# Kernel tuning notes

Hardware: AMD Instinct MI355X
Metric: run time of the kernel (lower is better)

## Reference

```python
import jax, jax.numpy as jnp
import numpy as np

B, L, LH, D, H = 32, 512, 2048, 1024, 4
DK = D // H  # dot-attn head dim
NEG = -1e9


def _ln(x, g, b, eps=1e-5):
    m = x.mean(-1, keepdims=True)
    v = ((x - m) ** 2).mean(-1, keepdims=True)
    return (x - m) / jnp.sqrt(v + eps) * g + b


def setup_inputs() -> dict:
    key = jax.random.key(0)
    ks = jax.random.split(key, 16)
    s = 0.05
    inp = {
        "seq_emb": jax.random.normal(ks[0], (B, L, D), jnp.float32),
        "seq_mask": jnp.ones((B, L), jnp.float32),
        "his_seq_emb": jax.random.normal(ks[1], (B, LH, D), jnp.float32),
        "his_seq_mask": jnp.ones((B, LH), jnp.float32),
        # dot-product MHA (bias=True)
        "sa_wq": jax.random.normal(ks[2], (D, D), jnp.float32) * s,
        "sa_bq": jnp.zeros((D,), jnp.float32),
        "sa_wk": jax.random.normal(ks[3], (D, D), jnp.float32) * s,
        "sa_bk": jnp.zeros((D,), jnp.float32),
        "sa_wv": jax.random.normal(ks[4], (D, D), jnp.float32) * s,
        "sa_bv": jnp.zeros((D,), jnp.float32),
        "sa_wo": jax.random.normal(ks[5], (D, D), jnp.float32) * s,
        "sa_bo": jnp.zeros((D,), jnp.float32),
        # short LayerNorm
        "sn_g": jnp.ones((D,), jnp.float32),
        "sn_b": jnp.zeros((D,), jnp.float32),
        # additive MHA (h=1, bias=False)
        "aa_wq": jax.random.normal(ks[6], (D, D), jnp.float32) * s,
        "aa_wk": jax.random.normal(ks[7], (D, D), jnp.float32) * s,
        "aa_wv": jax.random.normal(ks[8], (D, D), jnp.float32) * s,
        "aa_wo": jax.random.normal(ks[9], (D, D), jnp.float32) * s,
        "aa_wa": jax.random.normal(ks[10], (D,), jnp.float32) * s,
        # long LayerNorm
        "ln_g": jnp.ones((D,), jnp.float32),
        "ln_b": jnp.zeros((D,), jnp.float32),
    }
    return inp


def reference(seq_emb, seq_mask, his_seq_emb, his_seq_mask,
              sa_wq, sa_bq, sa_wk, sa_bk, sa_wv, sa_bv, sa_wo, sa_bo,
              sn_g, sn_b, aa_wq, aa_wk, aa_wv, aa_wo, aa_wa, ln_g, ln_b):
    # ---- dot-product self attention over seq_emb (dropout = eval/no-op) ----
    def split_heads(x):  # (B,L,D) -> (B,H,L,DK)
        return x.reshape(B, -1, H, DK).transpose(0, 2, 1, 3)

    q = split_heads(seq_emb @ sa_wq + sa_bq)
    k = split_heads(seq_emb @ sa_wk + sa_bk)
    v = split_heads(seq_emb @ sa_wv + sa_bv)
    scores = jnp.einsum('bhqd,bhkd->bhqk', q, k) / jnp.sqrt(jnp.float32(DK))
    scores = jnp.where(seq_mask[:, None, None, :] == 0, NEG, scores)
    p_attn = jax.nn.softmax(scores, axis=-1)  # (B,H,L,L)
    ctx = jnp.einsum('bhqk,bhkd->bhqd', p_attn, v)
    ctx = ctx.transpose(0, 2, 1, 3).reshape(B, L, D)
    sa_out = ctx @ sa_wo + sa_bo

    poi_attn = _ln(sa_out, sn_g, sn_b) * seq_mask[:, :, None]
    poi_hidden = poi_attn.mean(axis=1, keepdims=True)  # (B,1,D)

    # ---- additive (Bahdanau) attention, h=1, Lq=1 ----
    aq = poi_hidden @ aa_wq        # (B,1,D)
    ak = his_seq_emb @ aa_wk       # (B,LH,D)
    av = his_seq_emb @ aa_wv       # (B,LH,D)
    feats = jnp.tanh(aq[:, :, None, :] + ak[:, None, :, :])  # (B,1,LH,D)
    a_scores = jnp.einsum('bqkd,d->bqk', feats, aa_wa)        # (B,1,LH)
    a_scores = jnp.where(his_seq_mask[:, None, :] == 0, NEG, a_scores)
    a_w = jax.nn.softmax(a_scores, axis=-1)
    a_ctx = jnp.einsum('bqk,bkd->bqd', a_w, av)               # (B,1,D)
    aa_out = a_ctx @ aa_wo

    his_poi_hidden = poi_hidden + _ln(aa_out, ln_g, ln_b)     # (B,1,D)

    attn_weight = p_attn[:, 0, :, :]                          # (B,L,L)
    seq_hidden = jnp.concatenate([poi_hidden, his_poi_hidden], axis=-1)[:, 0, :]  # (B,2D)
    return seq_hidden, attn_weight
```

## Files before the change

kernel.cpp:

```cpp
#include <hip/hip_runtime.h>

#define NEGV (-1000000000.0f)

typedef __attribute__((ext_vector_type(8))) short sh8;
typedef __attribute__((ext_vector_type(4))) short sh4;
typedef __attribute__((ext_vector_type(8))) __bf16 bf16x8;
typedef __attribute__((ext_vector_type(4))) float f32x4;

__device__ __forceinline__ float b2f(unsigned short u) {
  unsigned v = ((unsigned)u) << 16;
  return __builtin_bit_cast(float, v);
}
__device__ __forceinline__ unsigned short f2b(float f) {
  unsigned x = __builtin_bit_cast(unsigned, f);
  unsigned r = (x + 0x7fffu + ((x >> 16) & 1u)) >> 16;
  return (unsigned short)r;
}
__device__ __forceinline__ void g2l16(const void* g, void* l) {
  __builtin_amdgcn_global_load_lds((const __attribute__((address_space(1))) unsigned int*)g,
                                   (__attribute__((address_space(3))) unsigned int*)l, 16, 0, 0);
}
__device__ __forceinline__ f32x4 mfma16(bf16x8 a, bf16x8 b, f32x4 c) {
  return __builtin_amdgcn_mfma_f32_16x16x32_bf16(a, b, c, 0, 0, 0);
}
__device__ __forceinline__ float fast_tanh(float x) {
  x = fminf(fmaxf(x, -15.f), 15.f);
  float e = __expf(2.f * x);
  return (e - 1.f) / (e + 1.f);
}

__global__ void cvt_bf16(const float* __restrict__ src, unsigned short* __restrict__ dst, int n4) {
  int i = blockIdx.x * blockDim.x + threadIdx.x;
  int stride = gridDim.x * blockDim.x;
  for (; i < n4; i += stride) {
    float4 v = ((const float4*)src)[i];
    sh4 o;
    o[0] = (short)f2b(v.x); o[1] = (short)f2b(v.y);
    o[2] = (short)f2b(v.z); o[3] = (short)f2b(v.w);
    ((sh4*)dst)[i] = o;
  }
}

__global__ void tcvt(const float* __restrict__ src, unsigned short* __restrict__ dst) {
  __shared__ float tile[64][65];
  int bx = blockIdx.x, by = blockIdx.y;
  int tx = threadIdx.x & 63, ty = threadIdx.x >> 6;
#pragma unroll
  for (int i = 0; i < 16; ++i) {
    int r = i * 4 + ty;
    tile[r][tx] = src[(size_t)(by * 64 + r) * 1024 + bx * 64 + tx];
  }
  __syncthreads();
#pragma unroll
  for (int i = 0; i < 16; ++i) {
    int r = i * 4 + ty;
    dst[(size_t)(bx * 64 + r) * 1024 + by * 64 + tx] = f2b(tile[tx][r]);
  }
}

template<int EPI>
__global__ __launch_bounds__(512, 1)
void gemm256(const unsigned short* __restrict__ A, const unsigned short* __restrict__ Bt,
             int nbx,
             const float* __restrict__ b0, const float* __restrict__ b1,
             const float* __restrict__ b2,
             unsigned short* __restrict__ O0, unsigned short* __restrict__ O1,
             unsigned short* __restrict__ O2,
             const float* __restrict__ aq, const float* __restrict__ wa,
             float* __restrict__ sc)
{
  __shared__ char lds[131072];
  const int tid = threadIdx.x;
  const int w = tid >> 6, l = tid & 63;
  const int wm = w >> 2, wn = w & 3;
  const int lr = l & 15, g = l >> 4;

  const int wg = blockIdx.x;
  const int cpx = gridDim.x >> 3;
  const int wgid = (wg & 7) * cpx + (wg >> 3);
  const int bx = wgid % nbx, by = wgid / nbx;
  const size_t m0 = (size_t)by * 256;
  const int n0 = bx * 256;

  f32x4 acc[8][4] = {};
  bf16x8 fa[4], fb[4];

  const int srow = w * 8 + (l >> 3);
  const int schunk = ((l & 7) ^ ((l >> 3) & 7)) * 8;
  const unsigned short* gA = A + (m0 + srow) * 1024 + schunk;
  const unsigned short* gB = Bt + ((size_t)n0 + srow) * 1024 + schunk;
  const int ldst = w * 1024;

  const int chs = lr & 7;
  const int aRd0 = wm * 16384 + lr * 128;
  const int bRd0 = 32768 + (wn >> 1) * 16384 + (wn & 1) * 8192 + lr * 128;
  const int ck0 = ((0 * 4 + g) ^ chs) * 16;
  const int ck1 = ((1 * 4 + g) ^ chs) * 16;

#define STG_A(BUF, AH, RH, KK) \
  g2l16(gA + ((AH) * 128 + (RH) * 64) * 1024 + (KK), \
        lds + (BUF) * 65536 + (AH) * 16384 + (RH) * 8192 + ldst)
#define STG_B(BUF, BH, RH, KK) \
  g2l16(gB + ((BH) * 128 + (RH) * 64) * 1024 + (KK), \
        lds + (BUF) * 65536 + 32768 + (BH) * 16384 + (RH) * 8192 + ldst)

#define PH(BUFOFF, CK, IH, STAGES, TAIL)                                      \
  {                                                                           \
    const char* pb_ = lds + (BUFOFF);                                         \
    if ((IH) == 0) {                                                          \
      _Pragma("unroll") for (int j = 0; j < 4; ++j)                           \
        fb[j] = *(const bf16x8*)(pb_ + bRd0 + j * 2048 + (CK));               \
    }                                                                         \
    _Pragma("unroll") for (int i = 0; i < 4; ++i)                             \
      fa[i] = *(const bf16x8*)(pb_ + aRd0 + (IH) * 8192 + i * 2048 + (CK));   \
    STAGES;                                                                   \
    __builtin_amdgcn_sched_barrier(0);                                        \
    asm volatile("s_barrier" ::: "memory");                                   \
    asm volatile("s_waitcnt lgkmcnt(0)" ::: "memory");                        \
    __builtin_amdgcn_sched_barrier(0);                                        \
    __builtin_amdgcn_s_setprio(1);                                            \
    _Pragma("unroll") for (int i = 0; i < 4; ++i)                             \
      _Pragma("unroll") for (int j = 0; j < 4; ++j)                           \
        acc[(IH) * 4 + i][j] = mfma16(fa[i], fb[j], acc[(IH) * 4 + i][j]);    \
    __builtin_amdgcn_s_setprio(0);                                            \
    TAIL;                                                                     \
    asm volatile("s_barrier" ::: "memory");                                   \
  }

  STG_A(0, 0, 0, 0); STG_A(0, 0, 1, 0); STG_A(0, 1, 0, 0); STG_A(0, 1, 1, 0);
  STG_B(0, 0, 0, 0); STG_B(0, 0, 1, 0); STG_B(0, 1, 0, 0); STG_B(0, 1, 1, 0);
  STG_A(1, 0, 0, 64); STG_A(1, 1, 0, 64);
  asm volatile("s_waitcnt vmcnt(0)" ::: "memory");
  asm volatile("s_barrier" ::: "memory");

#pragma unroll 1
  for (int t = 0; t < 8; ++t) {
    const int k1 = (2 * t + 1) * 64, k2 = (2 * t + 2) * 64, k3 = (2 * t + 3) * 64;
    const bool st = (t < 7);
    PH(0,     ck0, 0, { STG_A(1, 0, 1, k1); STG_A(1, 1, 1, k1); }, {})
    PH(0,     ck0, 1, { STG_B(1, 0, 0, k1); STG_B(1, 0, 1, k1); }, {})
    PH(0,     ck1, 0, { STG_B(1, 1, 0, k1); STG_B(1, 1, 1, k1); }, {})
    PH(0,     ck1, 1, { if (st) { STG_A(0, 0, 0, k2); STG_A(0, 1, 0, k2); } },
       { if (st) { asm volatile("s_waitcnt vmcnt(2)" ::: "memory"); }
         else    { asm volatile("s_waitcnt vmcnt(0)" ::: "memory"); } })
    PH(65536, ck0, 0, { if (st) { STG_A(0, 0, 1, k2); STG_A(0, 1, 1, k2); } }, {})
    PH(65536, ck0, 1, { if (st) { STG_B(0, 0, 0, k2); STG_B(0, 0, 1, k2); } }, {})
    PH(65536, ck1, 0, { if (st) { STG_B(0, 1, 0, k2); STG_B(0, 1, 1, k2); } }, {})
    PH(65536, ck1, 1, { if (st) { STG_A(1, 0, 0, k3); STG_A(1, 1, 0, k3); } },
       { if (st) { asm volatile("s_waitcnt vmcnt(2)" ::: "memory"); } })
  }
#undef PH
#undef STG_A
#undef STG_B

  if (EPI == 0) {
#pragma unroll
    for (int j = 0; j < 4; ++j) {
      int col = n0 + wn * 64 + j * 16 + lr;
      float bv = b0[col];
#pragma unroll
      for (int i = 0; i < 8; ++i) {
        size_t rowb = m0 + wm * 128 + i * 16 + g * 4;
#pragma unroll
        for (int r = 0; r < 4; ++r)
          O0[(rowb + r) * 1024 + col] = f2b(acc[i][j][r] + bv);
      }
    }
  } else if (EPI == 1) {
#pragma unroll
    for (int j = 0; j < 4; ++j) {
      int col3 = n0 + wn * 64 + j * 16 + lr;
      int part = col3 >> 10, c = col3 & 1023;
      float bv = (part == 0) ? b0[c] : (part == 1) ? b1[c] : b2[c];
      if (part < 2) {
        unsigned short* O = part == 0 ? O0 : O1;
#pragma unroll
        for (int i = 0; i < 8; ++i) {
          size_t rowb = m0 + wm * 128 + i * 16 + g * 4;
#pragma unroll
          for (int r = 0; r < 4; ++r)
            O[(rowb + r) * 1024 + c] = f2b(acc[i][j][r] + bv);
        }
      } else {
        int h = c >> 8, d = c & 255;
#pragma unroll
        for (int i = 0; i < 8; ++i) {
          size_t row = m0 + wm * 128 + i * 16 + g * 4;
          int bb = (int)(row >> 9), ll = (int)(row & 511);
          size_t base = ((size_t)(bb * 4 + h) * 256 + d) * 512 + ll;
#pragma unroll
          for (int r = 0; r < 4; ++r)
            O2[base + r] = f2b(acc[i][j][r] + bv);
        }
      }
    }
  } else {
    const int bb = (int)(m0 >> 11);
#pragma unroll
    for (int i = 0; i < 8; ++i) {
      float rp[4] = {0.f, 0.f, 0.f, 0.f};
#pragma unroll
      for (int j = 0; j < 4; ++j) {
        int col = n0 + wn * 64 + j * 16 + lr;
        float wav = wa[col];
        float aqv = aq[bb * 1024 + col];
#pragma unroll
        for (int r = 0; r < 4; ++r)
          rp[r] += wav * fast_tanh(acc[i][j][r] + aqv);
      }
#pragma unroll
      for (int off = 1; off < 16; off <<= 1)
#pragma unroll
        for (int r = 0; r < 4; ++r)
          rp[r] += __shfl_xor(rp[r], off, 64);
      if (lr == 0) {
        size_t rowb = m0 + wm * 128 + i * 16 + g * 4;
#pragma unroll
        for (int r = 0; r < 4; ++r)
          atomicAdd(&sc[rowb + r], rp[r]);
      }
    }
  }
}

__global__ __launch_bounds__(256, 4)
void attn_kernel(const unsigned short* __restrict__ q, const unsigned short* __restrict__ k,
                 const unsigned short* __restrict__ vT, const float* __restrict__ seq_mask,
                 unsigned short* __restrict__ ctx, float* __restrict__ attn_out)
{
  __shared__ char smem[34304];
  unsigned short* Qs = (unsigned short*)smem;
  unsigned short* Ps = (unsigned short*)smem;
  float* redm = (float*)(smem + 33280);
  float* reds = (float*)(smem + 33792);
  const int t = threadIdx.x, w = t >> 6, l = t & 63;
  const int lr = l & 15, g = l >> 4, lk8 = g * 8;
  const int wg = blockIdx.x;
  const int wgid = (wg & 7) * 256 + (wg >> 3);
  const int qt = wgid & 15, bh = wgid >> 4;
  const int h = bh & 3, b = bh >> 2;
  const int l0 = qt * 32;

  for (int idx = t; idx < 32 * 32; idx += 256) {
    int r = idx >> 5, ch = (idx & 31) * 8;
    *(sh8*)&Qs[r * 264 + ch] =
        *(const sh8*)&q[((size_t)(b * 512 + l0 + r)) * 1024 + h * 256 + ch];
  }
  __syncthreads();

  f32x4 accs[2][8] = {};
  const unsigned short* kbase = k + ((size_t)b * 512) * 1024 + h * 256;
#pragma unroll
  for (int ds = 0; ds < 8; ++ds) {
    int d0 = ds * 32;
    bf16x8 a0 = *(const bf16x8*)&Qs[lr * 264 + d0 + lk8];
    bf16x8 a1 = *(const bf16x8*)&Qs[(16 + lr) * 264 + d0 + lk8];
#pragma unroll
    for (int j = 0; j < 8; ++j) {
      int kj = w * 128 + j * 16 + lr;
      bf16x8 bb = *(const bf16x8*)&kbase[(size_t)kj * 1024 + d0 + lk8];
      accs[0][j] = mfma16(a0, bb, accs[0][j]);
      accs[1][j] = mfma16(a1, bb, accs[1][j]);
    }
  }

#pragma unroll
  for (int j = 0; j < 8; ++j) {
    int col = w * 128 + j * 16 + lr;
    float mv = seq_mask[b * 512 + col];
    bool msk = (mv == 0.f);
#pragma unroll
    for (int i = 0; i < 2; ++i)
#pragma unroll
      for (int r = 0; r < 4; ++r)
        accs[i][j][r] = msk ? NEGV : accs[i][j][r] * 0.0625f;
  }

  float mx[2][4], sm[2][4];
#pragma unroll
  for (int i = 0; i < 2; ++i)
#pragma unroll
    for (int r = 0; r < 4; ++r) {
      float m = accs[i][0][r];
#pragma unroll
      for (int j = 1; j < 8; ++j) m = fmaxf(m, accs[i][j][r]);
      mx[i][r] = m;
    }
#pragma unroll
  for (int off = 1; off < 16; off <<= 1)
#pragma unroll
    for (int i = 0; i < 2; ++i)
#pragma unroll
      for (int r = 0; r < 4; ++r)
        mx[i][r] = fmaxf(mx[i][r], __shfl_xor(mx[i][r], off, 64));
  if (lr == 0) {
#pragma unroll
    for (int i = 0; i < 2; ++i)
#pragma unroll
      for (int r = 0; r < 4; ++r)
        redm[w * 32 + i * 16 + g * 4 + r] = mx[i][r];
  }
  __syncthreads();
#pragma unroll
  for (int i = 0; i < 2; ++i)
#pragma unroll
    for (int r = 0; r < 4; ++r) {
      int row = i * 16 + g * 4 + r;
      mx[i][r] = fmaxf(fmaxf(redm[row], redm[32 + row]),
                       fmaxf(redm[64 + row], redm[96 + row]));
      sm[i][r] = 0.f;
    }

#pragma unroll
  for (int i = 0; i < 2; ++i)
#pragma unroll
    for (int j = 0; j < 8; ++j)
#pragma unroll
      for (int r = 0; r < 4; ++r) {
        float p = __expf(accs[i][j][r] - mx[i][r]);
        accs[i][j][r] = p;
        sm[i][r] += p;
      }
#pragma unroll
  for (int off = 1; off < 16; off <<= 1)
#pragma unroll
    for (int i = 0; i < 2; ++i)
#pragma unroll
      for (int r = 0; r < 4; ++r)
        sm[i][r] += __shfl_xor(sm[i][r], off, 64);
  if (lr == 0) {
#pragma unroll
    for (int i = 0; i < 2; ++i)
#pragma unroll
      for (int r = 0; r < 4; ++r)
        reds[w * 32 + i * 16 + g * 4 + r] = sm[i][r];
  }
  __syncthreads();
#pragma unroll
  for (int i = 0; i < 2; ++i)
#pragma unroll
    for (int r = 0; r < 4; ++r) {
      int row = i * 16 + g * 4 + r;
      float s = reds[row] + reds[32 + row] + reds[64 + row] + reds[96 + row];
      sm[i][r] = 1.f / s;
    }

#pragma unroll
  for (int i = 0; i < 2; ++i)
#pragma unroll
    for (int j = 0; j < 8; ++j) {
      int col = w * 128 + j * 16 + lr;
#pragma unroll
      for (int r = 0; r < 4; ++r) {
        int row = i * 16 + g * 4 + r;
        float pn = accs[i][j][r] * sm[i][r];
        Ps[row * 520 + col] = f2b(pn);
        if (h == 0)
          attn_out[((size_t)(b * 512 + l0 + row)) * 512 + col] = pn;
      }
    }
  __syncthreads();

  f32x4 acco[2][4] = {};
  const unsigned short* vbase = vT + ((size_t)(b * 4 + h)) * 256 * 512;
#pragma unroll
  for (int ks = 0; ks < 16; ++ks) {
    int kj0 = ks * 32;
    bf16x8 a0 = *(const bf16x8*)&Ps[lr * 520 + kj0 + lk8];
    bf16x8 a1 = *(const bf16x8*)&Ps[(16 + lr) * 520 + kj0 + lk8];
#pragma unroll
    for (int j = 0; j < 4; ++j) {
      int d = w * 64 + j * 16 + lr;
      bf16x8 bb = *(const bf16x8*)&vbase[(size_t)d * 512 + kj0 + lk8];
      acco[0][j] = mfma16(a0, bb, acco[0][j]);
      acco[1][j] = mfma16(a1, bb, acco[1][j]);
    }
  }
#pragma unroll
  for (int i = 0; i < 2; ++i)
#pragma unroll
    for (int j = 0; j < 4; ++j) {
      int col = w * 64 + j * 16 + lr;
#pragma unroll
      for (int r = 0; r < 4; ++r) {
        int row = i * 16 + g * 4 + r;
        ctx[((size_t)(b * 512 + l0 + row)) * 1024 + h * 256 + col] = f2b(acco[i][j][r]);
      }
    }
}

__global__ __launch_bounds__(256)
void ln_mean(const unsigned short* __restrict__ sa, const float* __restrict__ g,
             const float* __restrict__ bt, const float* __restrict__ mask,
             float* __restrict__ poi_sum)
{
  const int b = blockIdx.y, ch = blockIdx.x;
  const int t = threadIdx.x, w = t >> 6, l = t & 63;
  float gg[16], bb[16];
#pragma unroll
  for (int j = 0; j < 16; ++j) { gg[j] = g[l * 16 + j]; bb[j] = bt[l * 16 + j]; }
  float accv[16];
#pragma unroll
  for (int j = 0; j < 16; ++j) accv[j] = 0.f;
  for (int rr = 0; rr < 16; ++rr) {
    int row = ch * 64 + w * 16 + rr;
    const unsigned short* rp = sa + ((size_t)(b * 512 + row)) * 1024 + l * 16;
    float x[16];
    sh8 v0 = *(const sh8*)rp;
    sh8 v1 = *(const sh8*)(rp + 8);
#pragma unroll
    for (int j = 0; j < 8; ++j) {
      x[j] = b2f((unsigned short)v0[j]);
      x[8 + j] = b2f((unsigned short)v1[j]);
    }
    float s = 0.f, s2 = 0.f;
#pragma unroll
    for (int j = 0; j < 16; ++j) { s += x[j]; s2 += x[j] * x[j]; }
#pragma unroll
    for (int off = 1; off < 64; off <<= 1) {
      s += __shfl_xor(s, off, 64);
      s2 += __shfl_xor(s2, off, 64);
    }
    float mean = s * (1.f / 1024.f);
    float var = s2 * (1.f / 1024.f) - mean * mean;
    float rinv = rsqrtf(var + 1e-5f);
    float mk = mask[b * 512 + row];
#pragma unroll
    for (int j = 0; j < 16; ++j) accv[j] += ((x[j] - mean) * rinv * gg[j] + bb[j]) * mk;
  }
#pragma unroll
  for (int j = 0; j < 16; ++j) atomicAdd(&poi_sum[b * 1024 + l * 16 + j], accv[j]);
}

__global__ void finalize_poi(const float* __restrict__ ps, float* __restrict__ poi) {
  int i = blockIdx.x * 256 + threadIdx.x;
  if (i < 32 * 1024) poi[i] = ps[i] * (1.f / 512.f);
}

__global__ __launch_bounds__(256)
void gemv32(const float* __restrict__ in, const float* __restrict__ W, float* __restrict__ out)
{
  const int b = blockIdx.y;
  const int n = blockIdx.x * 256 + threadIdx.x;
  const float* ib = in + b * 1024;
  float acc = 0.f;
  for (int d = 0; d < 1024; d += 4) {
    acc += ib[d]     * W[(size_t)d * 1024 + n]
         + ib[d + 1] * W[(size_t)(d + 1) * 1024 + n]
         + ib[d + 2] * W[(size_t)(d + 2) * 1024 + n]
         + ib[d + 3] * W[(size_t)(d + 3) * 1024 + n];
  }
  out[b * 1024 + n] = acc;
}

__global__ __launch_bounds__(256)
void softmax_his(float* __restrict__ sc, const float* __restrict__ mask)
{
  __shared__ float red[4];
  const int b = blockIdx.x, t = threadIdx.x, w = t >> 6, l = t & 63;
  float v[8];
  float mx = -3.0e38f;
#pragma unroll
  for (int i = 0; i < 8; ++i) {
    int kk = t + i * 256;
    float s = (mask[b * 2048 + kk] == 0.f) ? NEGV : sc[b * 2048 + kk];
    v[i] = s;
    mx = fmaxf(mx, s);
  }
#pragma unroll
  for (int off = 1; off < 64; off <<= 1) mx = fmaxf(mx, __shfl_xor(mx, off, 64));
  if (l == 0) red[w] = mx;
  __syncthreads();
  mx = fmaxf(fmaxf(red[0], red[1]), fmaxf(red[2], red[3]));
  float sum = 0.f;
#pragma unroll
  for (int i = 0; i < 8; ++i) { v[i] = __expf(v[i] - mx); sum += v[i]; }
#pragma unroll
  for (int off = 1; off < 64; off <<= 1) sum += __shfl_xor(sum, off, 64);
  __syncthreads();
  if (l == 0) red[w] = sum;
  __syncthreads();
  sum = red[0] + red[1] + red[2] + red[3];
  float inv = 1.f / sum;
#pragma unroll
  for (int i = 0; i < 8; ++i) sc[b * 2048 + t + i * 256] = v[i] * inv;
}

__global__ __launch_bounds__(256)
void hw_kernel(const float* __restrict__ aw, const unsigned short* __restrict__ his,
               float* __restrict__ hw)
{
  const int b = blockIdx.y, kc = blockIdx.x, t = threadIdx.x;
  const int cb = t * 4;
  float a0 = 0.f, a1 = 0.f, a2 = 0.f, a3 = 0.f;
  for (int kk = 0; kk < 256; ++kk) {
    int k = kc * 256 + kk;
    float wg = aw[b * 2048 + k];
    sh4 vv = *(const sh4*)&his[((size_t)(b * 2048 + k)) * 1024 + cb];
    a0 += wg * b2f((unsigned short)vv[0]);
    a1 += wg * b2f((unsigned short)vv[1]);
    a2 += wg * b2f((unsigned short)vv[2]);
    a3 += wg * b2f((unsigned short)vv[3]);
  }
  atomicAdd(&hw[b * 1024 + cb + 0], a0);
  atomicAdd(&hw[b * 1024 + cb + 1], a1);
  atomicAdd(&hw[b * 1024 + cb + 2], a2);
  atomicAdd(&hw[b * 1024 + cb + 3], a3);
}

__global__ __launch_bounds__(256)
void final_kernel(const float* __restrict__ aa_out, const float* __restrict__ g,
                  const float* __restrict__ bt, const float* __restrict__ poi,
                  float* __restrict__ out)
{
  __shared__ float r1[4], r2[4];
  const int b = blockIdx.x, t = threadIdx.x, w = t >> 6, l = t & 63;
  float x[4];
#pragma unroll
  for (int j = 0; j < 4; ++j) x[j] = aa_out[b * 1024 + t * 4 + j];
  float s = 0.f, s2 = 0.f;
#pragma unroll
  for (int j = 0; j < 4; ++j) { s += x[j]; s2 += x[j] * x[j]; }
#pragma unroll
  for (int off = 1; off < 64; off <<= 1) {
    s += __shfl_xor(s, off, 64);
    s2 += __shfl_xor(s2, off, 64);
  }
  if (l == 0) { r1[w] = s; r2[w] = s2; }
  __syncthreads();
  s = r1[0] + r1[1] + r1[2] + r1[3];
  s2 = r2[0] + r2[1] + r2[2] + r2[3];
  float mean = s * (1.f / 1024.f);
  float var = s2 * (1.f / 1024.f) - mean * mean;
  float rinv = rsqrtf(var + 1e-5f);
#pragma unroll
  for (int j = 0; j < 4; ++j) {
    int c = t * 4 + j;
    float lnv = (x[j] - mean) * rinv * g[c] + bt[c];
    float pv = poi[b * 1024 + c];
    out[b * 2048 + c] = pv;
    out[b * 2048 + 1024 + c] = pv + lnv;
  }
}

extern "C" void kernel_launch(void* const* d_in, const int* in_sizes, int n_in,
                              void* d_out, int out_size, void* d_ws, size_t ws_size,
                              hipStream_t stream)
{
  const float* seq_emb  = (const float*)d_in[0];
  const float* seq_mask = (const float*)d_in[1];
  const float* his_emb  = (const float*)d_in[2];
  const float* his_mask = (const float*)d_in[3];
  const float* sa_wq = (const float*)d_in[4];
  const float* sa_bq = (const float*)d_in[5];
  const float* sa_wk = (const float*)d_in[6];
  const float* sa_bk = (const float*)d_in[7];
  const float* sa_wv = (const float*)d_in[8];
  const float* sa_bv = (const float*)d_in[9];
  const float* sa_wo = (const float*)d_in[10];
  const float* sa_bo = (const float*)d_in[11];
  const float* sn_g  = (const float*)d_in[12];
  const float* sn_b  = (const float*)d_in[13];
  const float* aa_wq = (const float*)d_in[14];
  const float* aa_wk = (const float*)d_in[15];
  const float* aa_wv = (const float*)d_in[16];
  const float* aa_wo = (const float*)d_in[17];
  const float* aa_wa = (const float*)d_in[18];
  const float* ln_g  = (const float*)d_in[19];
  const float* ln_b  = (const float*)d_in[20];
  float* out = (float*)d_out;

  char* p = (char*)d_ws;
  size_t off = 0;
  auto alloc = [&](size_t bytes) -> void* {
    void* r = p + off;
    off += (bytes + 255) & ~(size_t)255;
    return r;
  };
  unsigned short* seqb = (unsigned short*)alloc((size_t)16384 * 1024 * 2);
  unsigned short* hisb = (unsigned short*)alloc((size_t)65536 * 1024 * 2);
  unsigned short* wcat = (unsigned short*)alloc((size_t)3072 * 1024 * 2);
  unsigned short* woT  = (unsigned short*)alloc((size_t)1024 * 1024 * 2);
  unsigned short* awkT = (unsigned short*)alloc((size_t)1024 * 1024 * 2);
  unsigned short* qb   = (unsigned short*)alloc((size_t)16384 * 1024 * 2);
  unsigned short* kb   = (unsigned short*)alloc((size_t)16384 * 1024 * 2);
  unsigned short* vTb  = (unsigned short*)alloc((size_t)16384 * 1024 * 2);
  unsigned short* ctxb = (unsigned short*)alloc((size_t)16384 * 1024 * 2);
  unsigned short* saob = (unsigned short*)alloc((size_t)16384 * 1024 * 2);
  float* poi_sum = (float*)alloc((size_t)32 * 1024 * 4);
  float* poi     = (float*)alloc((size_t)32 * 1024 * 4);
  float* aqb     = (float*)alloc((size_t)32 * 1024 * 4);
  float* ascore  = (float*)alloc((size_t)32 * 2048 * 4);
  float* hwb     = (float*)alloc((size_t)32 * 1024 * 4);
  float* actx    = (float*)alloc((size_t)32 * 1024 * 4);
  float* aaout   = (float*)alloc((size_t)32 * 1024 * 4);
  if (off > ws_size) return;

  hipMemsetAsync(poi_sum, 0, (size_t)32 * 1024 * 4, stream);
  hipMemsetAsync(ascore, 0, (size_t)32 * 2048 * 4, stream);
  hipMemsetAsync(hwb, 0, (size_t)32 * 1024 * 4, stream);

  cvt_bf16<<<2048, 256, 0, stream>>>(seq_emb, seqb, 16384 * 1024 / 4);
  cvt_bf16<<<2048, 256, 0, stream>>>(his_emb, hisb, 65536 * 1024 / 4);
  dim3 tg(16, 16);
  tcvt<<<tg, 256, 0, stream>>>(sa_wq, wcat);
  tcvt<<<tg, 256, 0, stream>>>(sa_wk, wcat + (size_t)1024 * 1024);
  tcvt<<<tg, 256, 0, stream>>>(sa_wv, wcat + (size_t)2048 * 1024);
  tcvt<<<tg, 256, 0, stream>>>(sa_wo, woT);
  tcvt<<<tg, 256, 0, stream>>>(aa_wk, awkT);

  gemm256<1><<<768, 512, 0, stream>>>(seqb, wcat, 12, sa_bq, sa_bk, sa_bv,
                                      qb, kb, vTb, nullptr, nullptr, nullptr);

  attn_kernel<<<2048, 256, 0, stream>>>(qb, kb, vTb, seq_mask, ctxb, out + 65536);

  gemm256<0><<<256, 512, 0, stream>>>(ctxb, woT, 4, sa_bo, nullptr, nullptr,
                                      saob, nullptr, nullptr, nullptr, nullptr, nullptr);
  ln_mean<<<dim3(8, 32), 256, 0, stream>>>(saob, sn_g, sn_b, seq_mask, poi_sum);
  finalize_poi<<<128, 256, 0, stream>>>(poi_sum, poi);
  gemv32<<<dim3(4, 32), 256, 0, stream>>>(poi, aa_wq, aqb);

  gemm256<2><<<1024, 512, 0, stream>>>(hisb, awkT, 4, nullptr, nullptr, nullptr,
                                       nullptr, nullptr, nullptr, aqb, aa_wa, ascore);
  softmax_his<<<32, 256, 0, stream>>>(ascore, his_mask);
  hw_kernel<<<dim3(8, 32), 256, 0, stream>>>(ascore, hisb, hwb);
  gemv32<<<dim3(4, 32), 256, 0, stream>>>(hwb, aa_wv, actx);
  gemv32<<<dim3(4, 32), 256, 0, stream>>>(actx, aa_wo, aaout);
  final_kernel<<<32, 256, 0, stream>>>(aaout, ln_g, ln_b, poi, out);
}
```

Before: 784.3 us.

## Fuse fp32-to-bf16 activation conversion into GEMM A-tile loading

Removes the standalone cvt_bf16 passes over seq_emb and his_emb. A new gemm256f variant reads fp32 A tiles directly into registers, converts them to bf16 and writes them into swizzled LDS, pipelined alongside the async B loads. hw_kernel now reads fp32 his_emb directly. This avoids writing and re-reading large bf16 copies (about 384MB of extra traffic), but the GEMM now reads A at twice the bytes and routes it through registers instead of direct-to-LDS loads, which adds VGPR pressure and conversion ALU work to the main loop.

Result: slower. 906.7 us (+15.6%).

```diff
diff --git a/kernel.cpp b/kernel.cpp
--- a/kernel.cpp
+++ b/kernel.cpp
@@ -16,6 +16,14 @@
   unsigned r = (x + 0x7fffu + ((x >> 16) & 1u)) >> 16;
   return (unsigned short)r;
 }
+__device__ __forceinline__ sh8 cvt8(float4 a, float4 b) {
+  sh8 o;
+  o[0] = (short)f2b(a.x); o[1] = (short)f2b(a.y);
+  o[2] = (short)f2b(a.z); o[3] = (short)f2b(a.w);
+  o[4] = (short)f2b(b.x); o[5] = (short)f2b(b.y);
+  o[6] = (short)f2b(b.z); o[7] = (short)f2b(b.w);
+  return o;
+}
 __device__ __forceinline__ void g2l16(const void* g, void* l) {
   __builtin_amdgcn_global_load_lds((const __attribute__((address_space(1))) unsigned int*)g,
                                    (__attribute__((address_space(3))) unsigned int*)l, 16, 0, 0);
@@ -29,18 +37,6 @@
   return (e - 1.f) / (e + 1.f);
 }
 
-__global__ void cvt_bf16(const float* __restrict__ src, unsigned short* __restrict__ dst, int n4) {
-  int i = blockIdx.x * blockDim.x + threadIdx.x;
-  int stride = gridDim.x * blockDim.x;
-  for (; i < n4; i += stride) {
-    float4 v = ((const float4*)src)[i];
-    sh4 o;
-    o[0] = (short)f2b(v.x); o[1] = (short)f2b(v.y);
-    o[2] = (short)f2b(v.z); o[3] = (short)f2b(v.w);
-    ((sh4*)dst)[i] = o;
-  }
-}
-
 __global__ void tcvt(const float* __restrict__ src, unsigned short* __restrict__ dst) {
   __shared__ float tile[64][65];
   int bx = blockIdx.x, by = blockIdx.y;
@@ -58,16 +54,9 @@
   }
 }
 
-template<int EPI>
 __global__ __launch_bounds__(512, 1)
 void gemm256(const unsigned short* __restrict__ A, const unsigned short* __restrict__ Bt,
-             int nbx,
-             const float* __restrict__ b0, const float* __restrict__ b1,
-             const float* __restrict__ b2,
-             unsigned short* __restrict__ O0, unsigned short* __restrict__ O1,
-             unsigned short* __restrict__ O2,
-             const float* __restrict__ aq, const float* __restrict__ wa,
-             float* __restrict__ sc)
+             int nbx, const float* __restrict__ b0, unsigned short* __restrict__ O0)
 {
   __shared__ char lds[131072];
   const int tid = threadIdx.x;
@@ -153,20 +142,132 @@
 #undef STG_A
 #undef STG_B
 
-  if (EPI == 0) {
-#pragma unroll
-    for (int j = 0; j < 4; ++j) {
-      int col = n0 + wn * 64 + j * 16 + lr;
-      float bv = b0[col];
-#pragma unroll
-      for (int i = 0; i < 8; ++i) {
-        size_t rowb = m0 + wm * 128 + i * 16 + g * 4;
-#pragma unroll
-        for (int r = 0; r < 4; ++r)
-          O0[(rowb + r) * 1024 + col] = f2b(acc[i][j][r] + bv);
-      }
-    }
-  } else if (EPI == 1) {
+#pragma unroll
+  for (int j = 0; j < 4; ++j) {
+    int col = n0 + wn * 64 + j * 16 + lr;
+    float bv = b0[col];
+#pragma unroll
+    for (int i = 0; i < 8; ++i) {
+      size_t rowb = m0 + wm * 128 + i * 16 + g * 4;
+#pragma unroll
+      for (int r = 0; r < 4; ++r)
+        O0[(rowb + r) * 1024 + col] = f2b(acc[i][j][r] + bv);
+    }
+  }
+}
+
+template<int EPI>
+__global__ __launch_bounds__(512, 1)
+void gemm256f(const float* __restrict__ A, const unsigned short* __restrict__ Bt,
+              int nbx,
+              const float* __restrict__ b0, const float* __restrict__ b1,
+              const float* __restrict__ b2,
+              unsigned short* __restrict__ O0, unsigned short* __restrict__ O1,
+              unsigned short* __restrict__ O2,
+              const float* __restrict__ aq, const float* __restrict__ wa,
+              float* __restrict__ sc)
+{
+  __shared__ char lds[131072];
+  const int tid = threadIdx.x;
+  const int w = tid >> 6, l = tid & 63;
+  const int wm = w >> 2, wn = w & 3;
+  const int lr = l & 15, g = l >> 4;
+
+  const int wg = blockIdx.x;
+  const int cpx = gridDim.x >> 3;
+  const int wgid = (wg & 7) * cpx + (wg >> 3);
+  const int bx = wgid % nbx, by = wgid / nbx;
+  const size_t m0 = (size_t)by * 256;
+  const int n0 = bx * 256;
+
+  f32x4 acc[8][4] = {};
+  bf16x8 fa[4], fb[4];
+  float4 raL[4], raH[4];
+
+  const int ar = tid >> 3, ac = tid & 7;
+  const int acg = (ac ^ (ar & 7)) * 8;
+  const float* gAf = A + (m0 + ar) * 1024 + acg;
+  const int awr = ar * 128 + ac * 16;
+
+  const int srow = w * 8 + (l >> 3);
+  const int schunk = ((l & 7) ^ ((l >> 3) & 7)) * 8;
+  const unsigned short* gB = Bt + ((size_t)n0 + srow) * 1024 + schunk;
+  const int ldst = w * 1024;
+
+  const int chs = lr & 7;
+  const int aRd0 = wm * 16384 + lr * 128;
+  const int bRd0 = 32768 + (wn >> 1) * 16384 + (wn & 1) * 8192 + lr * 128;
+  const int ck0 = ((0 * 4 + g) ^ chs) * 16;
+  const int ck1 = ((1 * 4 + g) ^ chs) * 16;
+
+#define LDA(RV, RH, KK)                                                  \
+  { const float* s0_ = gAf + ((RH) * 64) * 1024 + (KK);                  \
+    RV[0] = *(const float4*)s0_;  RV[1] = *(const float4*)(s0_ + 4);     \
+    const float* s1_ = s0_ + 128 * 1024;                                 \
+    RV[2] = *(const float4*)s1_;  RV[3] = *(const float4*)(s1_ + 4); }
+#define WRA(BUF, RH, RV)                                                 \
+  { char* d0_ = lds + (BUF) * 65536 + (RH) * 8192 + awr;                 \
+    *(sh8*)d0_ = cvt8(RV[0], RV[1]);                                     \
+    *(sh8*)(d0_ + 16384) = cvt8(RV[2], RV[3]); }
+#define STG_B(BUF, BH, RH, KK) \
+  g2l16(gB + ((BH) * 128 + (RH) * 64) * 1024 + (KK), \
+        lds + (BUF) * 65536 + 32768 + (BH) * 16384 + (RH) * 8192 + ldst)
+
+#define PH(BUFOFF, CK, IH, STAGES, TAIL)                                      \
+  {                                                                           \
+    const char* pb_ = lds + (BUFOFF);                                         \
+    if ((IH) == 0) {                                                          \
+      _Pragma("unroll") for (int j = 0; j < 4; ++j)                           \
+        fb[j] = *(const bf16x8*)(pb_ + bRd0 + j * 2048 + (CK));               \
+    }                                                                         \
+    _Pragma("unroll") for (int i = 0; i < 4; ++i)                             \
+      fa[i] = *(const bf16x8*)(pb_ + aRd0 + (IH) * 8192 + i * 2048 + (CK));   \
+    STAGES;                                                                   \
+    __builtin_amdgcn_sched_barrier(0);                                        \
+    asm volatile("s_barrier" ::: "memory");                                   \
+    asm volatile("s_waitcnt lgkmcnt(0)" ::: "memory");                        \
+    __builtin_amdgcn_sched_barrier(0);                                        \
+    __builtin_amdgcn_s_setprio(1);                                            \
+    _Pragma("unroll") for (int i = 0; i < 4; ++i)                             \
+      _Pragma("unroll") for (int j = 0; j < 4; ++j)                           \
+        acc[(IH) * 4 + i][j] = mfma16(fa[i], fb[j], acc[(IH) * 4 + i][j]);    \
+    __builtin_amdgcn_s_setprio(0);                                            \
+    TAIL;                                                                     \
+    asm volatile("s_barrier" ::: "memory");                                   \
+  }
+
+  LDA(raL, 0, 0)
+  LDA(raH, 1, 0)
+  STG_B(0, 0, 0, 0); STG_B(0, 0, 1, 0); STG_B(0, 1, 0, 0); STG_B(0, 1, 1, 0);
+  WRA(0, 0, raL)
+  WRA(0, 1, raH)
+  LDA(raL, 0, 64)
+  asm volatile("s_waitcnt vmcnt(4)" ::: "memory");
+  asm volatile("s_waitcnt lgkmcnt(0)" ::: "memory");
+  asm volatile("s_barrier" ::: "memory");
+
+#pragma unroll 1
+  for (int t = 0; t < 8; ++t) {
+    const int k1 = (2 * t + 1) * 64, k2 = (2 * t + 2) * 64, k3 = (2 * t + 3) * 64;
+    const bool st = (t < 7);
+    PH(0,     ck0, 0, { LDA(raH, 1, k1) WRA(1, 0, raL) }, {})
+    PH(0,     ck0, 1, { STG_B(1, 0, 0, k1); STG_B(1, 0, 1, k1); }, {})
+    PH(0,     ck1, 0, { STG_B(1, 1, 0, k1); STG_B(1, 1, 1, k1); WRA(1, 1, raH) }, {})
+    PH(0,     ck1, 1, { if (st) { LDA(raL, 0, k2) } },
+       { if (st) { asm volatile("s_waitcnt vmcnt(4)" ::: "memory"); }
+         else    { asm volatile("s_waitcnt vmcnt(0)" ::: "memory"); } })
+    PH(65536, ck0, 0, { if (st) { LDA(raH, 1, k2) WRA(0, 0, raL) } }, {})
+    PH(65536, ck0, 1, { if (st) { STG_B(0, 0, 0, k2); STG_B(0, 0, 1, k2); } }, {})
+    PH(65536, ck1, 0, { if (st) { STG_B(0, 1, 0, k2); STG_B(0, 1, 1, k2); WRA(0, 1, raH) } }, {})
+    PH(65536, ck1, 1, { if (st) { LDA(raL, 0, k3) } },
+       { if (st) { asm volatile("s_waitcnt vmcnt(4)" ::: "memory"); } })
+  }
+#undef PH
+#undef LDA
+#undef WRA
+#undef STG_B
+
+  if (EPI == 1) {
 #pragma unroll
     for (int j = 0; j < 4; ++j) {
       int col3 = n0 + wn * 64 + j * 16 + lr;
@@ -487,7 +588,7 @@
 }
 
 __global__ __launch_bounds__(256)
-void hw_kernel(const float* __restrict__ aw, const unsigned short* __restrict__ his,
+void hw_kernel(const float* __restrict__ aw, const float* __restrict__ his,
                float* __restrict__ hw)
 {
   const int b = blockIdx.y, kc = blockIdx.x, t = threadIdx.x;
@@ -496,11 +597,11 @@
   for (int kk = 0; kk < 256; ++kk) {
     int k = kc * 256 + kk;
     float wg = aw[b * 2048 + k];
-    sh4 vv = *(const sh4*)&his[((size_t)(b * 2048 + k)) * 1024 + cb];
-    a0 += wg * b2f((unsigned short)vv[0]);
-    a1 += wg * b2f((unsigned short)vv[1]);
-    a2 += wg * b2f((unsigned short)vv[2]);
-    a3 += wg * b2f((unsigned short)vv[3]);
+    float4 vv = *(const float4*)&his[((size_t)(b * 2048 + k)) * 1024 + cb];
+    a0 += wg * vv.x;
+    a1 += wg * vv.y;
+    a2 += wg * vv.z;
+    a3 += wg * vv.w;
   }
   atomicAdd(&hw[b * 1024 + cb + 0], a0);
   atomicAdd(&hw[b * 1024 + cb + 1], a1);
@@ -577,8 +678,6 @@
     off += (bytes + 255) & ~(size_t)255;
     return r;
   };
-  unsigned short* seqb = (unsigned short*)alloc((size_t)16384 * 1024 * 2);
-  unsigned short* hisb = (unsigned short*)alloc((size_t)65536 * 1024 * 2);
   unsigned short* wcat = (unsigned short*)alloc((size_t)3072 * 1024 * 2);
   unsigned short* woT  = (unsigned short*)alloc((size_t)1024 * 1024 * 2);
   unsigned short* awkT = (unsigned short*)alloc((size_t)1024 * 1024 * 2);
@@ -600,8 +699,6 @@
   hipMemsetAsync(ascore, 0, (size_t)32 * 2048 * 4, stream);
   hipMemsetAsync(hwb, 0, (size_t)32 * 1024 * 4, stream);
 
-  cvt_bf16<<<2048, 256, 0, stream>>>(seq_emb, seqb, 16384 * 1024 / 4);
-  cvt_bf16<<<2048, 256, 0, stream>>>(his_emb, hisb, 65536 * 1024 / 4);
   dim3 tg(16, 16);
   tcvt<<<tg, 256, 0, stream>>>(sa_wq, wcat);
   tcvt<<<tg, 256, 0, stream>>>(sa_wk, wcat + (size_t)1024 * 1024);
@@ -609,21 +706,20 @@
   tcvt<<<tg, 256, 0, stream>>>(sa_wo, woT);
   tcvt<<<tg, 256, 0, stream>>>(aa_wk, awkT);
 
-  gemm256<1><<<768, 512, 0, stream>>>(seqb, wcat, 12, sa_bq, sa_bk, sa_bv,
-                                      qb, kb, vTb, nullptr, nullptr, nullptr);
+  gemm256f<1><<<768, 512, 0, stream>>>(seq_emb, wcat, 12, sa_bq, sa_bk, sa_bv,
+                                       qb, kb, vTb, nullptr, nullptr, nullptr);
 
   attn_kernel<<<2048, 256, 0, stream>>>(qb, kb, vTb, seq_mask, ctxb, out + 65536);
 
-  gemm256<0><<<256, 512, 0, stream>>>(ctxb, woT, 4, sa_bo, nullptr, nullptr,
-                                      saob, nullptr, nullptr, nullptr, nullptr, nullptr);
+  gemm256<<<256, 512, 0, stream>>>(ctxb, woT, 4, sa_bo, saob);
   ln_mean<<<dim3(8, 32), 256, 0, stream>>>(saob, sn_g, sn_b, seq_mask, poi_sum);
   finalize_poi<<<128, 256, 0, stream>>>(poi_sum, poi);
   gemv32<<<dim3(4, 32), 256, 0, stream>>>(poi, aa_wq, aqb);
 
-  gemm256<2><<<1024, 512, 0, stream>>>(hisb, awkT, 4, nullptr, nullptr, nullptr,
-                                       nullptr, nullptr, nullptr, aqb, aa_wa, ascore);
+  gemm256f<2><<<1024, 512, 0, stream>>>(his_emb, awkT, 4, nullptr, nullptr, nullptr,
+                                        nullptr, nullptr, nullptr, aqb, aa_wa, ascore);
   softmax_his<<<32, 256, 0, stream>>>(ascore, his_mask);
-  hw_kernel<<<dim3(8, 32), 256, 0, stream>>>(ascore, hisb, hwb);
+  hw_kernel<<<dim3(8, 32), 256, 0, stream>>>(ascore, his_emb, hwb);
   gemv32<<<dim3(4, 32), 256, 0, stream>>>(hwb, aa_wv, actx);
   gemv32<<<dim3(4, 32), 256, 0, stream>>>(actx, aa_wo, aaout);
   final_kernel<<<32, 256, 0, stream>>>(aaout, ln_g, ln_b, poi, out);
```
